# Kernel optimization log

Hardware: AMD Instinct MI355X
Metric: run time of the kernel (lower is better)

## Reference

```python
import jax, jax.numpy as jnp
import numpy as np

NODE_DIM = 64
EDGE_DIM = 16
HIDDEN = 64
INPUT_DIM = 2 * NODE_DIM + EDGE_DIM  # 144
NEG_SLOPE = 0.1
LN_EPS = 1e-5


def _layer_norm(x, gamma, beta):
    mu = jnp.mean(x, axis=-1, keepdims=True)
    var = jnp.var(x, axis=-1, keepdims=True)
    return (x - mu) * jax.lax.rsqrt(var + LN_EPS) * gamma + beta


def _leaky_relu(x):
    return jnp.where(x >= 0, x, NEG_SLOPE * x)


def setup_inputs() -> dict:
    key = jax.random.key(0)
    ks = jax.random.split(key, 10)
    n_nodes, n_edges = 50000, 1600000
    node_features = jax.random.normal(ks[0], (n_nodes, NODE_DIM), dtype=jnp.float32)
    edge_index = jax.random.randint(ks[1], (2, n_edges), 0, n_nodes, dtype=jnp.int64)
    edge_attr = jax.random.normal(ks[2], (n_edges, EDGE_DIM), dtype=jnp.float32)
    # MLP parameters (kaiming-ish scale)
    W1 = jax.random.normal(ks[3], (INPUT_DIM, HIDDEN), dtype=jnp.float32) / np.sqrt(INPUT_DIM)
    b1 = jnp.zeros((HIDDEN,), dtype=jnp.float32)
    g1 = jnp.ones((HIDDEN,), dtype=jnp.float32)
    be1 = jnp.zeros((HIDDEN,), dtype=jnp.float32)
    W2 = jax.random.normal(ks[4], (HIDDEN, HIDDEN), dtype=jnp.float32) / np.sqrt(HIDDEN)
    b2 = jnp.zeros((HIDDEN,), dtype=jnp.float32)
    g2 = jnp.ones((HIDDEN,), dtype=jnp.float32)
    be2 = jnp.zeros((HIDDEN,), dtype=jnp.float32)
    W3 = jax.random.normal(ks[5], (HIDDEN, 1), dtype=jnp.float32) / np.sqrt(HIDDEN)
    b3 = jnp.zeros((1,), dtype=jnp.float32)
    return {
        "node_features": node_features, "edge_index": edge_index, "edge_attr": edge_attr,
        "W1": W1, "b1": b1, "g1": g1, "be1": be1,
        "W2": W2, "b2": b2, "g2": g2, "be2": be2,
        "W3": W3, "b3": b3,
    }


def reference(node_features, edge_index, edge_attr,
              W1, b1, g1, be1, W2, b2, g2, be2, W3, b3):
    src = node_features[edge_index[0]]  # (E, node_dim)
    dst = node_features[edge_index[1]]  # (E, node_dim)
    x = jnp.concatenate([src, dst, edge_attr], axis=-1)  # (E, input_dim)
    h = _leaky_relu(_layer_norm(x @ W1 + b1, g1, be1))
    h = _leaky_relu(_layer_norm(h @ W2 + b2, g2, be2))
    return (h @ W3 + b3)[:, 0]  # (E,) logits
```

## Files before the change

### kernel.cpp

```cpp
#include <hip/hip_runtime.h>
#include <stdint.h>


#define TPB 256
#define NEG_SLOPE 0.1f
#define LN_EPS    1e-5f

typedef __attribute__((ext_vector_type(8))) short short8;
typedef __attribute__((ext_vector_type(4))) float f32x4;

__device__ __forceinline__ uint32_t fb(float x) {
  union { float f; uint32_t u; } c; c.f = x; return c.u;
}
__device__ __forceinline__ float bf(uint32_t x) {
  union { uint32_t u; float f; } c; c.u = x; return c.f;
}
__device__ __forceinline__ uint32_t cvtpk(float a, float b) {
  uint32_t r; asm("v_cvt_pk_bf16_f32 %0, %1, %2" : "=v"(r) : "v"(a), "v"(b));
  return r;
}
__device__ __forceinline__ short8 cvt8(f32x4 a, f32x4 b) {
  union { short8 s; uint32_t u[4]; } r;
  r.u[0] = cvtpk(a[0], a[1]);
  r.u[1] = cvtpk(a[2], a[3]);
  r.u[2] = cvtpk(b[0], b[1]);
  r.u[3] = cvtpk(b[2], b[3]);
  return r.s;
}
__device__ __forceinline__ short bf16rne(float x) {
  uint32_t u = fb(x);
  return (short)((u + 0x7fffu + ((u >> 16) & 1u)) >> 16);
}

template <int CTRL>
__device__ __forceinline__ float dppadd(float v) {
  int r = __builtin_amdgcn_update_dpp(0, (int)fb(v), CTRL, 0xf, 0xf, true);
  return v + bf((uint32_t)r);
}
__device__ __forceinline__ float rowsum16(float v) {
  v = dppadd<0x121>(v);
  v = dppadd<0x122>(v);
  v = dppadd<0x124>(v);
  v = dppadd<0x128>(v);
  return v;
}
__device__ __forceinline__ void redsum16(f32x4& v) {
  #pragma unroll
  for (int c = 0; c < 4; ++c) v[c] = rowsum16(v[c]);
}

__device__ __forceinline__ void lnstats(const f32x4& a0, const f32x4& a1,
                                        const f32x4& a2, const f32x4& a3,
                                        f32x4& mu, f32x4& rs) {
  f32x4 sv = a0 + a1 + a2 + a3;
  f32x4 qv = a0 * a0 + a1 * a1 + a2 * a2 + a3 * a3;
  redsum16(sv);
  redsum16(qv);
  mu = sv * (1.f / 64.f);
  f32x4 var = qv * (1.f / 64.f) - mu * mu;
  rs[0] = rsqrtf(var[0] + LN_EPS); rs[1] = rsqrtf(var[1] + LN_EPS);
  rs[2] = rsqrtf(var[2] + LN_EPS); rs[3] = rsqrtf(var[3] + LN_EPS);
}

#define SW1 168
#define SW2 72

__global__ __launch_bounds__(TPB, 3)
void edge_mlp_mfma(const float* __restrict__ nf, const int* __restrict__ ei,
                   const float* __restrict__ ea,
                   const float* __restrict__ W1, const float* __restrict__ b1,
                   const float* __restrict__ g1, const float* __restrict__ be1,
                   const float* __restrict__ W2, const float* __restrict__ b2,
                   const float* __restrict__ g2, const float* __restrict__ be2,
                   const float* __restrict__ W3, const float* __restrict__ b3,
                   float* __restrict__ out, int E, int ntiles) {
  __shared__ short W1T[64 * SW1];
  __shared__ short W2T[64 * SW2];
  __shared__ short HB[4][16 * SW2];

  const int tid  = threadIdx.x;
  const int lane = tid & 63;
  const int wv   = tid >> 6;
  const int ln   = lane & 15;
  const int quad = lane >> 4;

  for (int i = tid; i < 9216; i += TPB) {
    int n = i & 63, k = i >> 6;
    W1T[n * SW1 + k] = bf16rne(W1[k * 64 + n]);
  }
  for (int i = tid; i < 1024; i += TPB) {
    int n = i & 63, k = 144 + (i >> 6);
    W1T[n * SW1 + k] = 0;
  }
  for (int i = tid; i < 4096; i += TPB) {
    int n = i & 63, k = i >> 6;
    W2T[n * SW2 + k] = bf16rne(W2[k * 64 + n]);
  }
  __syncthreads();

  float b1v[4], g1v[4], be1v[4], b2v[4], g2v[4], be2v[4], W3v[4];
  #pragma unroll
  for (int jt = 0; jt < 4; ++jt) {
    int n = ln + 16 * jt;
    b1v[jt] = b1[n];  g1v[jt] = g1[n];  be1v[jt] = be1[n];
    b2v[jt] = b2[n];  g2v[jt] = g2[n];  be2v[jt] = be2[n];
    W3v[jt] = W3[n];
  }
  const float b3s = b3[0];

  const bool idx64 = (__ballot(ei[2 * lane + 1] == 0) == ~0ull);

  int sI[4], dI[4], sN[4], dN[4];
  {
    const int eb0 = blockIdx.x * 256 + wv * 64;
    #pragma unroll
    for (int mt = 0; mt < 4; ++mt) {
      int el = eb0 + mt * 16 + ln;
      int ec = el < E ? el : E - 1;
      if (idx64) { sI[mt] = ei[2 * ec]; dI[mt] = ei[2 * (E + ec)]; }
      else       { sI[mt] = ei[ec];     dI[mt] = ei[E + ec]; }
      sN[mt] = sI[mt]; dN[mt] = dI[mt];
    }
  }

  f32x4 raw[10];
  auto issue = [&](int s, int d, int el) {
    int ec = el < E ? el : E - 1;
    const float* sp = nf + (size_t)s * 64 + quad * 8;
    const float* dp = nf + (size_t)d * 64 + quad * 8;
    const float* ap = ea + (size_t)ec * 16 + (quad & 1) * 8;
    raw[0] = *(const f32x4*)sp;        raw[1] = *(const f32x4*)(sp + 4);
    raw[2] = *(const f32x4*)(sp + 32); raw[3] = *(const f32x4*)(sp + 36);
    raw[4] = *(const f32x4*)dp;        raw[5] = *(const f32x4*)(dp + 4);
    raw[6] = *(const f32x4*)(dp + 32); raw[7] = *(const f32x4*)(dp + 36);
    raw[8] = *(const f32x4*)ap;        raw[9] = *(const f32x4*)(ap + 4);
  };

  issue(sI[0], dI[0], blockIdx.x * 256 + wv * 64 + ln);

  for (int tile = blockIdx.x; tile < ntiles; tile += gridDim.x) {
    const int ebase = tile * 256 + wv * 64;

    #pragma unroll
    for (int mt = 0; mt < 4; ++mt) {
      short8 afr[5];
      afr[0] = cvt8(raw[0], raw[1]);
      afr[1] = cvt8(raw[2], raw[3]);
      afr[2] = cvt8(raw[4], raw[5]);
      afr[3] = cvt8(raw[6], raw[7]);
      afr[4] = cvt8(raw[8], raw[9]);

      f32x4 acc[4];
      #pragma unroll
      for (int jt = 0; jt < 4; ++jt) acc[jt] = (f32x4)(b1v[jt]);

      #pragma unroll
      for (int t = 0; t < 5; ++t)
        #pragma unroll
        for (int jt = 0; jt < 4; ++jt) {
          short8 bfr = *(const short8*)&W1T[(jt * 16 + ln) * SW1 + t * 32 + quad * 8];
          acc[jt] = __builtin_amdgcn_mfma_f32_16x16x32_bf16(
              afr[t], bfr, acc[jt], 0, 0, 0);
        }

      if (mt == 1) {
        int ntile = tile + gridDim.x;
        if (ntile < ntiles) {
          const int nb = ntile * 256 + wv * 64;
          #pragma unroll
          for (int m2 = 0; m2 < 4; ++m2) {
            int el = nb + m2 * 16 + ln;
            int ec = el < E ? el : E - 1;
            if (idx64) { sN[m2] = ei[2 * ec]; dN[m2] = ei[2 * (E + ec)]; }
            else       { sN[m2] = ei[ec];     dN[m2] = ei[E + ec]; }
          }
        }
      }

      if (mt < 3) issue(sI[mt + 1], dI[mt + 1], ebase + (mt + 1) * 16 + ln);
      else        issue(sN[0], dN[0], (tile + (int)gridDim.x) * 256 + wv * 64 + ln);

      f32x4 mu, rs;
      lnstats(acc[0], acc[1], acc[2], acc[3], mu, rs);

      #pragma unroll
      for (int jt = 0; jt < 4; ++jt)
        #pragma unroll
        for (int r = 0; r < 4; ++r) {
          float h = (acc[jt][r] - mu[r]) * rs[r] * g1v[jt] + be1v[jt];
          h = fmaxf(h, NEG_SLOPE * h);
          HB[wv][(quad * 4 + r) * SW2 + ln + 16 * jt] = (short)cvtpk(h, h);
        }

      f32x4 acc2[4];
      #pragma unroll
      for (int jt = 0; jt < 4; ++jt) acc2[jt] = (f32x4)(b2v[jt]);
      #pragma unroll
      for (int t2 = 0; t2 < 2; ++t2) {
        short8 a2 = *(const short8*)&HB[wv][ln * SW2 + t2 * 32 + quad * 8];
        #pragma unroll
        for (int jt = 0; jt < 4; ++jt) {
          short8 w2f = *(const short8*)&W2T[(jt * 16 + ln) * SW2 + t2 * 32 + quad * 8];
          acc2[jt] = __builtin_amdgcn_mfma_f32_16x16x32_bf16(
              a2, w2f, acc2[jt], 0, 0, 0);
        }
      }

      f32x4 mu2, rs2;
      lnstats(acc2[0], acc2[1], acc2[2], acc2[3], mu2, rs2);

      f32x4 po = (f32x4)0.f;
      #pragma unroll
      for (int jt = 0; jt < 4; ++jt)
        #pragma unroll
        for (int r = 0; r < 4; ++r) {
          float h = (acc2[jt][r] - mu2[r]) * rs2[r] * g2v[jt] + be2v[jt];
          h = fmaxf(h, NEG_SLOPE * h);
          po[r] = fmaf(h, W3v[jt], po[r]);
        }
      redsum16(po);

      if (ln < 4) {
        int e = ebase + mt * 16 + quad * 4 + ln;
        if (e < E) {
          float v = (ln == 0) ? po[0] : (ln == 1) ? po[1]
                  : (ln == 2) ? po[2] : po[3];
          out[e] = v + b3s;
        }
      }
    }

    #pragma unroll
    for (int m2 = 0; m2 < 4; ++m2) { sI[m2] = sN[m2]; dI[m2] = dN[m2]; }
  }
}

extern "C" void kernel_launch(void* const* d_in, const int* in_sizes, int n_in,
                              void* d_out, int out_size, void* d_ws, size_t ws_size,
                              hipStream_t stream) {
  const float* nf = (const float*)d_in[0];
  const int*   ei = (const int*)d_in[1];
  const float* ea = (const float*)d_in[2];

  const int E = out_size;
  const int ntiles = (E + 255) / 256;
  const int blocks = ntiles < 2048 ? ntiles : 2048;

  edge_mlp_mfma<<<blocks, TPB, 0, stream>>>(
      nf, ei, ea,
      (const float*)d_in[3],  (const float*)d_in[4],
      (const float*)d_in[5],  (const float*)d_in[6],
      (const float*)d_in[7],  (const float*)d_in[8],
      (const float*)d_in[9],  (const float*)d_in[10],
      (const float*)d_in[11], (const float*)d_in[12],
      (float*)d_out, E, ntiles);
}
```

Measured before the change: 291.3 us.

## Pre-convert node features to bf16 in workspace and gather bf16 rows

```diff
diff --git a/kernel.cpp b/kernel.cpp
--- a/kernel.cpp
+++ b/kernel.cpp
@@ -65,15 +65,210 @@
 #define SW1 168
 #define SW2 72
 
+__global__ __launch_bounds__(256)
+void cvt_nf(const float* __restrict__ nf, unsigned short* __restrict__ nfb,
+            int n) {
+  int i = (blockIdx.x * 256 + threadIdx.x) * 8;
+  if (i < n) {
+    f32x4 a = *(const f32x4*)(nf + i);
+    f32x4 b = *(const f32x4*)(nf + i + 4);
+    union { short8 s; uint32_t u[4]; } r;
+    r.u[0] = cvtpk(a[0], a[1]); r.u[1] = cvtpk(a[2], a[3]);
+    r.u[2] = cvtpk(b[0], b[1]); r.u[3] = cvtpk(b[2], b[3]);
+    *(short8*)(nfb + i) = r.s;
+  }
+}
+
+__global__ __launch_bounds__(TPB, 4)
+void edge_mlp_mfma_bf(const unsigned short* __restrict__ nfb,
+                      const int* __restrict__ ei,
+                      const float* __restrict__ ea,
+                      const float* __restrict__ W1, const float* __restrict__ b1,
+                      const float* __restrict__ g1, const float* __restrict__ be1,
+                      const float* __restrict__ W2, const float* __restrict__ b2,
+                      const float* __restrict__ g2, const float* __restrict__ be2,
+                      const float* __restrict__ W3, const float* __restrict__ b3,
+                      float* __restrict__ out, int E, int ntiles) {
+  __shared__ short W1T[64 * SW1];
+  __shared__ short W2T[64 * SW2];
+  __shared__ short HB[4][16 * SW2];
+
+  const int tid  = threadIdx.x;
+  const int lane = tid & 63;
+  const int wv   = tid >> 6;
+  const int ln   = lane & 15;
+  const int quad = lane >> 4;
+
+  for (int i = tid; i < 9216; i += TPB) {
+    int n = i & 63, k = i >> 6;
+    W1T[n * SW1 + k] = bf16rne(W1[k * 64 + n]);
+  }
+  for (int i = tid; i < 1024; i += TPB) {
+    int n = i & 63, k = 144 + (i >> 6);
+    W1T[n * SW1 + k] = 0;
+  }
+  for (int i = tid; i < 4096; i += TPB) {
+    int n = i & 63, k = i >> 6;
+    W2T[n * SW2 + k] = bf16rne(W2[k * 64 + n]);
+  }
+  __syncthreads();
+
+  float b1v[4], b2v[4], W3v[4];
+  uint32_t gb1v[4], gb2v[4];
+  #pragma unroll
+  for (int jt = 0; jt < 4; ++jt) {
+    int n = ln + 16 * jt;
+    b1v[jt] = b1[n];  b2v[jt] = b2[n];  W3v[jt] = W3[n];
+    gb1v[jt] = ((uint32_t)(unsigned short)bf16rne(g1[n]) << 16)
+             | (unsigned short)bf16rne(be1[n]);
+    gb2v[jt] = ((uint32_t)(unsigned short)bf16rne(g2[n]) << 16)
+             | (unsigned short)bf16rne(be2[n]);
+  }
+  const float b3s = b3[0];
+
+  const bool idx64 = (__ballot(ei[2 * lane + 1] == 0) == ~0ull);
+
+  int sI[4], dI[4], sN[4], dN[4];
+  {
+    const int eb0 = blockIdx.x * 256 + wv * 64;
+    #pragma unroll
+    for (int mt = 0; mt < 4; ++mt) {
+      int el = eb0 + mt * 16 + ln;
+      int ec = el < E ? el : E - 1;
+      if (idx64) { sI[mt] = ei[2 * ec]; dI[mt] = ei[2 * (E + ec)]; }
+      else       { sI[mt] = ei[ec];     dI[mt] = ei[E + ec]; }
+      sN[mt] = sI[mt]; dN[mt] = dI[mt];
+    }
+  }
+
+  short8 gbank[2][4];
+  f32x4  ebank[2][2];
+  auto issueG = [&](int bank, int s, int d, int el) {
+    int ec = el < E ? el : E - 1;
+    const unsigned short* sp = nfb + (size_t)s * 64 + quad * 8;
+    const unsigned short* dp = nfb + (size_t)d * 64 + quad * 8;
+    const float* ap = ea + (size_t)ec * 16 + (quad & 1) * 8;
+    gbank[bank][0] = *(const short8*)sp;
+    gbank[bank][1] = *(const short8*)(sp + 32);
+    gbank[bank][2] = *(const short8*)dp;
+    gbank[bank][3] = *(const short8*)(dp + 32);
+    ebank[bank][0] = *(const f32x4*)ap;
+    ebank[bank][1] = *(const f32x4*)(ap + 4);
+  };
+
+  issueG(0, sI[0], dI[0], blockIdx.x * 256 + wv * 64 + ln);
+
+  for (int tile = blockIdx.x; tile < ntiles; tile += gridDim.x) {
+    const int ebase = tile * 256 + wv * 64;
+
+    #pragma unroll
+    for (int mt = 0; mt < 4; ++mt) {
+      const int cur = mt & 1, nxt = cur ^ 1;
+
+      short8 afr4 = cvt8(ebank[cur][0], ebank[cur][1]);
+
+      f32x4 acc[4];
+      #pragma unroll
+      for (int jt = 0; jt < 4; ++jt) acc[jt] = (f32x4)(b1v[jt]);
+
+      #pragma unroll
+      for (int t = 0; t < 5; ++t) {
+        short8 af = (t < 4) ? gbank[cur][t] : afr4;
+        #pragma unroll
+        for (int jt = 0; jt < 4; ++jt) {
+          short8 bfr = *(const short8*)&W1T[(jt * 16 + ln) * SW1 + t * 32 + quad * 8];
+          acc[jt] = __builtin_amdgcn_mfma_f32_16x16x32_bf16(
+              af, bfr, acc[jt], 0, 0, 0);
+        }
+      }
+
+      if (mt == 1) {
+        int ntile = tile + gridDim.x;
+        if (ntile < ntiles) {
+          const int nb = ntile * 256 + wv * 64;
+          #pragma unroll
+          for (int m2 = 0; m2 < 4; ++m2) {
+            int el = nb + m2 * 16 + ln;
+            int ec = el < E ? el : E - 1;
+            if (idx64) { sN[m2] = ei[2 * ec]; dN[m2] = ei[2 * (E + ec)]; }
+            else       { sN[m2] = ei[ec];     dN[m2] = ei[E + ec]; }
+          }
+        }
+      }
+
+      if (mt < 3) issueG(nxt, sI[mt + 1], dI[mt + 1], ebase + (mt + 1) * 16 + ln);
+      else        issueG(nxt, sN[0], dN[0], (tile + (int)gridDim.x) * 256 + wv * 64 + ln);
+
+      f32x4 mu, rs;
+      lnstats(acc[0], acc[1], acc[2], acc[3], mu, rs);
+
+      #pragma unroll
+      for (int jt = 0; jt < 4; ++jt) {
+        float gA = bf(gb1v[jt] & 0xffff0000u);
+        float bA = bf((uint32_t)(gb1v[jt] << 16));
+        #pragma unroll
+        for (int r = 0; r < 4; ++r) {
+          float h = (acc[jt][r] - mu[r]) * rs[r] * gA + bA;
+          h = fmaxf(h, NEG_SLOPE * h);
+          HB[wv][(quad * 4 + r) * SW2 + ln + 16 * jt] = (short)cvtpk(h, h);
+        }
+      }
+
+      f32x4 acc2[4];
+      #pragma unroll
+      for (int jt = 0; jt < 4; ++jt) acc2[jt] = (f32x4)(b2v[jt]);
+      #pragma unroll
+      for (int t2 = 0; t2 < 2; ++t2) {
+        short8 a2 = *(const short8*)&HB[wv][ln * SW2 + t2 * 32 + quad * 8];
+        #pragma unroll
+        for (int jt = 0; jt < 4; ++jt) {
+          short8 w2f = *(const short8*)&W2T[(jt * 16 + ln) * SW2 + t2 * 32 + quad * 8];
+          acc2[jt] = __builtin_amdgcn_mfma_f32_16x16x32_bf16(
+              a2, w2f, acc2[jt], 0, 0, 0);
+        }
+      }
+
+      f32x4 mu2, rs2;
+      lnstats(acc2[0], acc2[1], acc2[2], acc2[3], mu2, rs2);
+
+      f32x4 po = (f32x4)0.f;
+      #pragma unroll
+      for (int jt = 0; jt < 4; ++jt) {
+        float gA = bf(gb2v[jt] & 0xffff0000u);
+        float bA = bf((uint32_t)(gb2v[jt] << 16));
+        #pragma unroll
+        for (int r = 0; r < 4; ++r) {
+          float h = (acc2[jt][r] - mu2[r]) * rs2[r] * gA + bA;
+          h = fmaxf(h, NEG_SLOPE * h);
+          po[r] = fmaf(h, W3v[jt], po[r]);
+        }
+      }
+      redsum16(po);
+
+      if (ln < 4) {
+        int e = ebase + mt * 16 + quad * 4 + ln;
+        if (e < E) {
+          float v = (ln == 0) ? po[0] : (ln == 1) ? po[1]
+                  : (ln == 2) ? po[2] : po[3];
+          out[e] = v + b3s;
+        }
+      }
+    }
+
+    #pragma unroll
+    for (int m2 = 0; m2 < 4; ++m2) { sI[m2] = sN[m2]; dI[m2] = dN[m2]; }
+  }
+}
+
 __global__ __launch_bounds__(TPB, 3)
-void edge_mlp_mfma(const float* __restrict__ nf, const int* __restrict__ ei,
-                   const float* __restrict__ ea,
-                   const float* __restrict__ W1, const float* __restrict__ b1,
-                   const float* __restrict__ g1, const float* __restrict__ be1,
-                   const float* __restrict__ W2, const float* __restrict__ b2,
-                   const float* __restrict__ g2, const float* __restrict__ be2,
-                   const float* __restrict__ W3, const float* __restrict__ b3,
-                   float* __restrict__ out, int E, int ntiles) {
+void edge_mlp_mfma_f32(const float* __restrict__ nf, const int* __restrict__ ei,
+                       const float* __restrict__ ea,
+                       const float* __restrict__ W1, const float* __restrict__ b1,
+                       const float* __restrict__ g1, const float* __restrict__ be1,
+                       const float* __restrict__ W2, const float* __restrict__ b2,
+                       const float* __restrict__ g2, const float* __restrict__ be2,
+                       const float* __restrict__ W3, const float* __restrict__ b3,
+                       float* __restrict__ out, int E, int ntiles) {
   __shared__ short W1T[64 * SW1];
   __shared__ short W2T[64 * SW2];
   __shared__ short HB[4][16 * SW2];
@@ -246,12 +441,29 @@
   const int ntiles = (E + 255) / 256;
   const int blocks = ntiles < 2048 ? ntiles : 2048;
 
-  edge_mlp_mfma<<<blocks, TPB, 0, stream>>>(
-      nf, ei, ea,
-      (const float*)d_in[3],  (const float*)d_in[4],
-      (const float*)d_in[5],  (const float*)d_in[6],
-      (const float*)d_in[7],  (const float*)d_in[8],
-      (const float*)d_in[9],  (const float*)d_in[10],
-      (const float*)d_in[11], (const float*)d_in[12],
-      (float*)d_out, E, ntiles);
-}
+  const size_t nfElems = (size_t)in_sizes[0];
+  const bool useWS = (d_ws != nullptr) &&
+                     (ws_size >= nfElems * sizeof(unsigned short));
+
+  if (useWS) {
+    const int cblk = (int)((nfElems / 8 + 255) / 256);
+    cvt_nf<<<cblk, 256, 0, stream>>>(nf, (unsigned short*)d_ws, (int)nfElems);
+    edge_mlp_mfma_bf<<<blocks, TPB, 0, stream>>>(
+        (const unsigned short*)d_ws, ei, ea,
+        (const float*)d_in[3],  (const float*)d_in[4],
+        (const float*)d_in[5],  (const float*)d_in[6],
+        (const float*)d_in[7],  (const float*)d_in[8],
+        (const float*)d_in[9],  (const float*)d_in[10],
+        (const float*)d_in[11], (const float*)d_in[12],
+        (float*)d_out, E, ntiles);
+  } else {
+    edge_mlp_mfma_f32<<<blocks, TPB, 0, stream>>>(
+        nf, ei, ea,
+        (const float*)d_in[3],  (const float*)d_in[4],
+        (const float*)d_in[5],  (const float*)d_in[6],
+        (const float*)d_in[7],  (const float*)d_in[8],
+        (const float*)d_in[9],  (const float*)d_in[10],
+        (const float*)d_in[11], (const float*)d_in[12],
+        (float*)d_out, E, ntiles);
+  }
+}
```

New measurement: 287.5 us. Within noise of the previous version (-1.3%).
